# Kernel tuning notes

Measured on AMD Instinct MI355X. Metric: run time of the kernel, lower is better.

The kernel has to match this reference:

```python
import jax, jax.numpy as jnp
import numpy as np

NUM_CAPSULE = 10
DIM_CAPSULE = 16
NUM_ROUTING = 3
EPS = 1e-7  # tf.keras.backend.epsilon()


def squash(v, axis=-1):
    s2 = jnp.sum(jnp.square(v), axis=axis, keepdims=True)
    scale = s2 / (1.0 + s2) / jnp.sqrt(s2 + EPS)
    return scale * v


def setup_inputs() -> dict:
    key = jax.random.key(0)
    k1, k2 = jax.random.split(key)
    B, in_dim = 16384, 2048
    inputs = jax.random.normal(k1, (B, in_dim), dtype=jnp.float32)
    # glorot-uniform-ish scale for the kernel
    limit = np.sqrt(6.0 / (in_dim + NUM_CAPSULE * DIM_CAPSULE)).astype(np.float32)
    kernel = jax.random.uniform(k2, (in_dim, NUM_CAPSULE * DIM_CAPSULE),
                                dtype=jnp.float32, minval=-limit, maxval=limit)
    return {"inputs": inputs, "kernel": kernel}


def reference(inputs, kernel):
    B = inputs.shape[0]
    # [B, in_dim] @ [in_dim, nc*dc] -> [B, nc, dc]
    inputs_hat = (inputs @ kernel).reshape(B, NUM_CAPSULE, DIM_CAPSULE)
    b = jnp.zeros((B, NUM_CAPSULE, 1), dtype=inputs.dtype)
    outputs = None
    for _ in range(NUM_ROUTING):
        c = jax.nn.softmax(b, axis=1)                      # [B, nc, 1]
        s = jnp.sum(c * inputs_hat, axis=1, keepdims=True)  # [B, 1, dc]
        outputs = squash(s)                                 # [B, 1, dc]
        # matmul(inputs_hat, outputs, transpose_b=True) -> [B, nc, 1]
        b = b + jnp.einsum('bnd,bd->bn', inputs_hat, outputs[:, 0, :])[:, :, None]
    return outputs[:, 0, :]  # [B, dc]
```

## Files before the change

kernel.cpp:

```cpp
#include <hip/hip_runtime.h>

typedef unsigned int u32;
typedef unsigned short u16;
typedef __attribute__((ext_vector_type(8))) __bf16 bf16x8;
typedef __attribute__((ext_vector_type(4))) float f32x4;

#define N_CAP 10
#define D_CAP 16
#define NN 160
#define KK 2048
#define BM 64
#define NSTEPS 64
#define THREADS 704
#define HAT_STRIDE 165
#define BSTEP 20480
#define TILE_B 8192
#define NBUF 3

__device__ __align__(16) unsigned char Wpack_g[NSTEPS * BSTEP];

__device__ __forceinline__ u32 pack_hi(float f0, float f1) {
  u32 u0 = __builtin_bit_cast(u32, f0), u1 = __builtin_bit_cast(u32, f1);
  return (u0 >> 16) | (u1 & 0xFFFF0000u);
}
__device__ __forceinline__ float hi_part(float f) {
  u32 u = __builtin_bit_cast(u32, f) & 0xFFFF0000u;
  return __builtin_bit_cast(float, u);
}
union U4B8 { uint4 u; bf16x8 b; };

__device__ __forceinline__ void split2(const float4& x, const float4& y,
                                       bf16x8& h, bf16x8& l) {
  U4B8 hh, ll;
  hh.u.x = pack_hi(x.x, x.y); hh.u.y = pack_hi(x.z, x.w);
  hh.u.z = pack_hi(y.x, y.y); hh.u.w = pack_hi(y.z, y.w);
  float l0 = x.x - hi_part(x.x), l1 = x.y - hi_part(x.y);
  float l2 = x.z - hi_part(x.z), l3 = x.w - hi_part(x.w);
  float l4 = y.x - hi_part(y.x), l5 = y.y - hi_part(y.y);
  float l6 = y.z - hi_part(y.z), l7 = y.w - hi_part(y.w);
  ll.u.x = pack_hi(l0, l1); ll.u.y = pack_hi(l2, l3);
  ll.u.z = pack_hi(l4, l5); ll.u.w = pack_hi(l6, l7);
  h = hh.b; l = ll.b;
}

__global__ void pack_w(const float* __restrict__ W) {
  const int tid = blockIdx.x * 256 + threadIdx.x;
  if (tid >= NSTEPS * 5 * 64 * 4) return;
  const int v = tid & 3;
  const int lane = (tid >> 2) & 63;
  const int sw = tid >> 8;
  const int wjp = sw % 5;
  const int s = sw / 5;
  const int col = 32 * wjp + 16 * (v & 1) + (lane & 15);
  const int kb = 32 * s + 8 * (lane >> 4);
  u32 r[4];
#pragma unroll
  for (int jj = 0; jj < 4; ++jj) {
    float x0 = W[(size_t)(kb + 2 * jj) * NN + col];
    float x1 = W[(size_t)(kb + 2 * jj + 1) * NN + col];
    if (v >= 2) { x0 -= hi_part(x0); x1 -= hi_part(x1); }
    r[jj] = pack_hi(x0, x1);
  }
  uint4 o; o.x = r[0]; o.y = r[1]; o.z = r[2]; o.w = r[3];
  *(uint4*)(Wpack_g + (size_t)tid * 16) = o;
}

#define GLOAD(gp, lp) __builtin_amdgcn_global_load_lds( \
    (const __attribute__((address_space(1))) u32*)(gp), \
    (__attribute__((address_space(3))) u32*)(lp), 16, 0, 0)
#define BARRIER() asm volatile("s_barrier" ::: "memory")

__global__ __launch_bounds__(THREADS, 1) void capsule_fused(
    const float* __restrict__ X, float* __restrict__ out) {
  __shared__ __align__(16) char smem[BM * HAT_STRIDE * 4];
  char* As = smem;
  float* hat = (float*)smem;

  const int t = threadIdx.x;
  const int rbase = blockIdx.x * BM;
  const int lane = t & 63;
  const int w = t >> 6;

  if (w == 10) {
    const float* g0 = X + (size_t)(rbase + (lane >> 3)) * KK
                        + (size_t)(((lane & 7) ^ (lane >> 3)) * 4);
#define STAGE(sv, bv) do {                                        \
    const float* gs_ = g0 + (size_t)(sv) * 32;                    \
    char* lb_ = As + (bv) * TILE_B;                               \
    GLOAD(gs_,           lb_);                                    \
    GLOAD(gs_ +  8 * KK, lb_ + 1024);                             \
    GLOAD(gs_ + 16 * KK, lb_ + 2048);                             \
    GLOAD(gs_ + 24 * KK, lb_ + 3072);                             \
    GLOAD(gs_ + 32 * KK, lb_ + 4096);                             \
    GLOAD(gs_ + 40 * KK, lb_ + 5120);                             \
    GLOAD(gs_ + 48 * KK, lb_ + 6144);                             \
    GLOAD(gs_ + 56 * KK, lb_ + 7168);                             \
  } while (0)
    STAGE(0, 0);
    STAGE(1, 1);
    asm volatile("s_waitcnt vmcnt(8)" ::: "memory");
    BARRIER();
    int pj = 2;
#pragma unroll 1
    for (int s = 0; s < NSTEPS; ++s) {
      if (s + 2 < NSTEPS) {
        STAGE(s + 2, pj);
        asm volatile("s_waitcnt vmcnt(8)" ::: "memory");
      } else {
        asm volatile("s_waitcnt vmcnt(0)" ::: "memory");
      }
      BARRIER();
      pj = (pj == 2) ? 0 : pj + 1;
    }
#undef STAGE
  } else {
    const int wip = (w >= 5) ? 1 : 0;
    const int wjp = w - 5 * wip;
    const int l15 = lane & 15;
    const int q = lane >> 4;
    const int r0 = 32 * wip + l15;
    const int r1 = r0 + 16;
    const int c0 = 2 * q, c1 = 2 * q + 1;
    const int o00 = (r0 >> 3) * 1024 + (r0 & 7) * 128 + ((c0 ^ (r0 & 7)) << 4);
    const int o01 = (r0 >> 3) * 1024 + (r0 & 7) * 128 + ((c1 ^ (r0 & 7)) << 4);
    const int o10 = (r1 >> 3) * 1024 + (r1 & 7) * 128 + ((c0 ^ (r1 & 7)) << 4);
    const int o11 = (r1 >> 3) * 1024 + (r1 & 7) * 128 + ((c1 ^ (r1 & 7)) << 4);
    const unsigned char* pB = Wpack_g + ((size_t)(wjp * 64 + lane)) * 64;

    f32x4 acc00 = {0.f,0.f,0.f,0.f}, acc01 = {0.f,0.f,0.f,0.f};
    f32x4 acc10 = {0.f,0.f,0.f,0.f}, acc11 = {0.f,0.f,0.f,0.f};

    BARRIER();
    int ci = 0;
#pragma unroll 1
    for (int s = 0; s < NSTEPS; ++s) {
      const uint4* bp4 = (const uint4*)(pB + (size_t)s * BSTEP);
      uint4 B0 = bp4[0], B1 = bp4[1], B2 = bp4[2], B3 = bp4[3];
      const char* cb = As + ci * TILE_B;
      float4 A00 = *(const float4*)(cb + o00);
      float4 A01 = *(const float4*)(cb + o01);
      float4 A10 = *(const float4*)(cb + o10);
      float4 A11 = *(const float4*)(cb + o11);
      bf16x8 ah0, al0, ah1, al1;
      split2(A00, A01, ah0, al0);
      split2(A10, A11, ah1, al1);
      U4B8 ub0, ub1, ub2, ub3;
      ub0.u = B0; ub1.u = B1; ub2.u = B2; ub3.u = B3;
      acc00 = __builtin_amdgcn_mfma_f32_16x16x32_bf16(ah0, ub0.b, acc00, 0,0,0);
      acc00 = __builtin_amdgcn_mfma_f32_16x16x32_bf16(ah0, ub2.b, acc00, 0,0,0);
      acc00 = __builtin_amdgcn_mfma_f32_16x16x32_bf16(al0, ub0.b, acc00, 0,0,0);
      acc01 = __builtin_amdgcn_mfma_f32_16x16x32_bf16(ah0, ub1.b, acc01, 0,0,0);
      acc01 = __builtin_amdgcn_mfma_f32_16x16x32_bf16(ah0, ub3.b, acc01, 0,0,0);
      acc01 = __builtin_amdgcn_mfma_f32_16x16x32_bf16(al0, ub1.b, acc01, 0,0,0);
      acc10 = __builtin_amdgcn_mfma_f32_16x16x32_bf16(ah1, ub0.b, acc10, 0,0,0);
      acc10 = __builtin_amdgcn_mfma_f32_16x16x32_bf16(ah1, ub2.b, acc10, 0,0,0);
      acc10 = __builtin_amdgcn_mfma_f32_16x16x32_bf16(al1, ub0.b, acc10, 0,0,0);
      acc11 = __builtin_amdgcn_mfma_f32_16x16x32_bf16(ah1, ub1.b, acc11, 0,0,0);
      acc11 = __builtin_amdgcn_mfma_f32_16x16x32_bf16(ah1, ub3.b, acc11, 0,0,0);
      acc11 = __builtin_amdgcn_mfma_f32_16x16x32_bf16(al1, ub1.b, acc11, 0,0,0);
      BARRIER();
      ci = (ci == 2) ? 0 : ci + 1;
    }
#pragma unroll
    for (int r = 0; r < 4; ++r) {
      const int rowb = 32 * wip + 4 * q + r;
      const int colb = 32 * wjp + l15;
      hat[rowb * HAT_STRIDE + colb]             = acc00[r];
      hat[rowb * HAT_STRIDE + colb + 16]        = acc01[r];
      hat[(rowb + 16) * HAT_STRIDE + colb]      = acc10[r];
      hat[(rowb + 16) * HAT_STRIDE + colb + 16] = acc11[r];
    }
  }
  __syncthreads();

  if (t < BM * 8) {
    const int r = t >> 3;
    const int d0 = t & 7;
    float h0[N_CAP], h1[N_CAP];
#pragma unroll
    for (int n = 0; n < N_CAP; ++n) {
      h0[n] = hat[r * HAT_STRIDE + n * D_CAP + d0];
      h1[n] = hat[r * HAT_STRIDE + n * D_CAP + d0 + 8];
    }
    float bb[N_CAP];
#pragma unroll
    for (int n = 0; n < N_CAP; ++n) bb[n] = 0.f;
    float v0 = 0.f, v1 = 0.f;
#pragma unroll
    for (int it = 0; it < 3; ++it) {
      float mx = bb[0];
#pragma unroll
      for (int n = 1; n < N_CAP; ++n) mx = fmaxf(mx, bb[n]);
      float c[N_CAP], se = 0.f;
#pragma unroll
      for (int n = 0; n < N_CAP; ++n) { c[n] = __expf(bb[n] - mx); se += c[n]; }
      const float inv = 1.f / se;
      float s0 = 0.f, s1 = 0.f;
#pragma unroll
      for (int n = 0; n < N_CAP; ++n) { s0 += c[n] * h0[n]; s1 += c[n] * h1[n]; }
      s0 *= inv; s1 *= inv;
      float s2 = s0 * s0 + s1 * s1;
      s2 += __shfl_xor(s2, 1);
      s2 += __shfl_xor(s2, 2);
      s2 += __shfl_xor(s2, 4);
      const float scale = s2 / ((1.f + s2) * sqrtf(s2 + 1e-7f));
      v0 = scale * s0; v1 = scale * s1;
      if (it < 2) {
#pragma unroll
        for (int n = 0; n < N_CAP; ++n) {
          float dd = h0[n] * v0 + h1[n] * v1;
          dd += __shfl_xor(dd, 1);
          dd += __shfl_xor(dd, 2);
          dd += __shfl_xor(dd, 4);
          bb[n] += dd;
        }
      }
    }
    out[(size_t)(rbase + r) * D_CAP + d0] = v0;
    out[(size_t)(rbase + r) * D_CAP + d0 + 8] = v1;
  }
}

extern "C" void kernel_launch(void* const* d_in, const int* in_sizes, int n_in,
                              void* d_out, int out_size, void* d_ws, size_t ws_size,
                              hipStream_t stream) {
  const float* X = (const float*)d_in[0];
  const float* W = (const float*)d_in[1];
  if (n_in >= 2 && in_sizes[0] == KK * NN) {
    X = (const float*)d_in[1];
    W = (const float*)d_in[0];
  }
  (void)d_ws; (void)ws_size; (void)out_size;
  pack_w<<<(NSTEPS * 5 * 64 * 4 + 255) / 256, 256, 0, stream>>>(W);
  capsule_fused<<<16384 / BM, THREADS, 0, stream>>>(X, (float*)d_out);
}
```

Measured before the change: 239.4 us.

## Double K-step per barrier and register-prefetch packed weights one iteration ahead

```diff
diff --git a/kernel.cpp b/kernel.cpp
--- a/kernel.cpp
+++ b/kernel.cpp
@@ -11,10 +11,11 @@
 #define KK 2048
 #define BM 64
 #define NSTEPS 64
+#define NITER 32
 #define THREADS 704
 #define HAT_STRIDE 165
 #define BSTEP 20480
-#define TILE_B 8192
+#define TILE2 16384
 #define NBUF 3
 
 __device__ __align__(16) unsigned char Wpack_g[NSTEPS * BSTEP];
@@ -69,12 +70,13 @@
     (const __attribute__((address_space(1))) u32*)(gp), \
     (__attribute__((address_space(3))) u32*)(lp), 16, 0, 0)
 #define BARRIER() asm volatile("s_barrier" ::: "memory")
+#define BLOAD(dst, addr) \
+  asm volatile("global_load_dwordx4 %0, %1, off" : "=v"(dst) : "v"(addr))
 
 __global__ __launch_bounds__(THREADS, 1) void capsule_fused(
     const float* __restrict__ X, float* __restrict__ out) {
-  __shared__ __align__(16) char smem[BM * HAT_STRIDE * 4];
-  char* As = smem;
-  float* hat = (float*)smem;
+  __shared__ __align__(16) char As[NBUF * TILE2];
+  __shared__ __align__(16) float hat[BM * HAT_STRIDE];
 
   const int t = threadIdx.x;
   const int rbase = blockIdx.x * BM;
@@ -84,35 +86,45 @@
   if (w == 10) {
     const float* g0 = X + (size_t)(rbase + (lane >> 3)) * KK
                         + (size_t)(((lane & 7) ^ (lane >> 3)) * 4);
-#define STAGE(sv, bv) do {                                        \
-    const float* gs_ = g0 + (size_t)(sv) * 32;                    \
-    char* lb_ = As + (bv) * TILE_B;                               \
-    GLOAD(gs_,           lb_);                                    \
-    GLOAD(gs_ +  8 * KK, lb_ + 1024);                             \
-    GLOAD(gs_ + 16 * KK, lb_ + 2048);                             \
-    GLOAD(gs_ + 24 * KK, lb_ + 3072);                             \
-    GLOAD(gs_ + 32 * KK, lb_ + 4096);                             \
-    GLOAD(gs_ + 40 * KK, lb_ + 5120);                             \
-    GLOAD(gs_ + 48 * KK, lb_ + 6144);                             \
-    GLOAD(gs_ + 56 * KK, lb_ + 7168);                             \
+#define STAGE2(IT, BV) do {                                       \
+    const float* ga_ = g0 + (size_t)(2 * (IT)) * 32;              \
+    char* la_ = As + (BV) * TILE2;                                \
+    GLOAD(ga_,           la_);                                    \
+    GLOAD(ga_ +  8 * KK, la_ + 1024);                             \
+    GLOAD(ga_ + 16 * KK, la_ + 2048);                             \
+    GLOAD(ga_ + 24 * KK, la_ + 3072);                             \
+    GLOAD(ga_ + 32 * KK, la_ + 4096);                             \
+    GLOAD(ga_ + 40 * KK, la_ + 5120);                             \
+    GLOAD(ga_ + 48 * KK, la_ + 6144);                             \
+    GLOAD(ga_ + 56 * KK, la_ + 7168);                             \
+    const float* gb_ = ga_ + 32;                                  \
+    char* lb_ = la_ + 8192;                                       \
+    GLOAD(gb_,           lb_);                                    \
+    GLOAD(gb_ +  8 * KK, lb_ + 1024);                             \
+    GLOAD(gb_ + 16 * KK, lb_ + 2048);                             \
+    GLOAD(gb_ + 24 * KK, lb_ + 3072);                             \
+    GLOAD(gb_ + 32 * KK, lb_ + 4096);                             \
+    GLOAD(gb_ + 40 * KK, lb_ + 5120);                             \
+    GLOAD(gb_ + 48 * KK, lb_ + 6144);                             \
+    GLOAD(gb_ + 56 * KK, lb_ + 7168);                             \
   } while (0)
-    STAGE(0, 0);
-    STAGE(1, 1);
-    asm volatile("s_waitcnt vmcnt(8)" ::: "memory");
+    STAGE2(0, 0);
+    STAGE2(1, 1);
+    asm volatile("s_waitcnt vmcnt(16)" ::: "memory");
     BARRIER();
     int pj = 2;
 #pragma unroll 1
-    for (int s = 0; s < NSTEPS; ++s) {
-      if (s + 2 < NSTEPS) {
-        STAGE(s + 2, pj);
-        asm volatile("s_waitcnt vmcnt(8)" ::: "memory");
+    for (int i = 0; i < NITER; ++i) {
+      if (i + 2 < NITER) {
+        STAGE2(i + 2, pj);
+        asm volatile("s_waitcnt vmcnt(16)" ::: "memory");
       } else {
         asm volatile("s_waitcnt vmcnt(0)" ::: "memory");
       }
       BARRIER();
       pj = (pj == 2) ? 0 : pj + 1;
     }
-#undef STAGE
+#undef STAGE2
   } else {
     const int wip = (w >= 5) ? 1 : 0;
     const int wjp = w - 5 * wip;
@@ -125,42 +137,75 @@
     const int o01 = (r0 >> 3) * 1024 + (r0 & 7) * 128 + ((c1 ^ (r0 & 7)) << 4);
     const int o10 = (r1 >> 3) * 1024 + (r1 & 7) * 128 + ((c0 ^ (r1 & 7)) << 4);
     const int o11 = (r1 >> 3) * 1024 + (r1 & 7) * 128 + ((c1 ^ (r1 & 7)) << 4);
-    const unsigned char* pB = Wpack_g + ((size_t)(wjp * 64 + lane)) * 64;
+    const unsigned char* pBw = Wpack_g + ((size_t)(wjp * 64 + lane)) * 64;
 
     f32x4 acc00 = {0.f,0.f,0.f,0.f}, acc01 = {0.f,0.f,0.f,0.f};
     f32x4 acc10 = {0.f,0.f,0.f,0.f}, acc11 = {0.f,0.f,0.f,0.f};
 
+    uint4 Ba[8], Bb[8];
+    BLOAD(Ba[0], pBw);                BLOAD(Ba[1], pBw + 16);
+    BLOAD(Ba[2], pBw + 32);           BLOAD(Ba[3], pBw + 48);
+    BLOAD(Ba[4], pBw + BSTEP);        BLOAD(Ba[5], pBw + BSTEP + 16);
+    BLOAD(Ba[6], pBw + BSTEP + 32);   BLOAD(Ba[7], pBw + BSTEP + 48);
+
     BARRIER();
     int ci = 0;
+
+#define MFMA12(AH0, AL0, AH1, AL1, B0, B1, B2, B3)                               \
+    {                                                                            \
+      U4B8 u0, u1, u2, u3;                                                       \
+      u0.u = B0; u1.u = B1; u2.u = B2; u3.u = B3;                                \
+      acc00 = __builtin_amdgcn_mfma_f32_16x16x32_bf16(AH0, u0.b, acc00, 0,0,0);  \
+      acc00 = __builtin_amdgcn_mfma_f32_16x16x32_bf16(AH0, u2.b, acc00, 0,0,0);  \
+      acc00 = __builtin_amdgcn_mfma_f32_16x16x32_bf16(AL0, u0.b, acc00, 0,0,0);  \
+      acc01 = __builtin_amdgcn_mfma_f32_16x16x32_bf16(AH0, u1.b, acc01, 0,0,0);  \
+      acc01 = __builtin_amdgcn_mfma_f32_16x16x32_bf16(AH0, u3.b, acc01, 0,0,0);  \
+      acc01 = __builtin_amdgcn_mfma_f32_16x16x32_bf16(AL0, u1.b, acc01, 0,0,0);  \
+      acc10 = __builtin_amdgcn_mfma_f32_16x16x32_bf16(AH1, u0.b, acc10, 0,0,0);  \
+      acc10 = __builtin_amdgcn_mfma_f32_16x16x32_bf16(AH1, u2.b, acc10, 0,0,0);  \
+      acc10 = __builtin_amdgcn_mfma_f32_16x16x32_bf16(AL1, u0.b, acc10, 0,0,0);  \
+      acc11 = __builtin_amdgcn_mfma_f32_16x16x32_bf16(AH1, u1.b, acc11, 0,0,0);  \
+      acc11 = __builtin_amdgcn_mfma_f32_16x16x32_bf16(AH1, u3.b, acc11, 0,0,0);  \
+      acc11 = __builtin_amdgcn_mfma_f32_16x16x32_bf16(AL1, u1.b, acc11, 0,0,0);  \
+    }
+
+#define ITER(I, BC, BN)                                                          \
+    {                                                                            \
+      const char* cb = As + ci * TILE2;                                          \
+      float4 A00a = *(const float4*)(cb + o00);                                  \
+      float4 A01a = *(const float4*)(cb + o01);                                  \
+      float4 A10a = *(const float4*)(cb + o10);                                  \
+      float4 A11a = *(const float4*)(cb + o11);                                  \
+      float4 A00b = *(const float4*)(cb + 8192 + o00);                           \
+      float4 A01b = *(const float4*)(cb + 8192 + o01);                           \
+      float4 A10b = *(const float4*)(cb + 8192 + o10);                           \
+      float4 A11b = *(const float4*)(cb + 8192 + o11);                           \
+      const unsigned char* bp = pBw + (size_t)((((I) + 1) & (NITER - 1)) * 2) * BSTEP; \
+      BLOAD(BN[0], bp);              BLOAD(BN[1], bp + 16);                      \
+      BLOAD(BN[2], bp + 32);         BLOAD(BN[3], bp + 48);                      \
+      BLOAD(BN[4], bp + BSTEP);      BLOAD(BN[5], bp + BSTEP + 16);              \
+      BLOAD(BN[6], bp + BSTEP + 32); BLOAD(BN[7], bp + BSTEP + 48);              \
+      bf16x8 ah0a, al0a, ah1a, al1a, ah0b, al0b, ah1b, al1b;                     \
+      split2(A00a, A01a, ah0a, al0a);                                            \
+      split2(A10a, A11a, ah1a, al1a);                                            \
+      split2(A00b, A01b, ah0b, al0b);                                            \
+      split2(A10b, A11b, ah1b, al1b);                                            \
+      asm volatile("s_waitcnt vmcnt(8)" ::: "memory");           \
+      __builtin_amdgcn_sched_barrier(0);                                         \
+      MFMA12(ah0a, al0a, ah1a, al1a, BC[0], BC[1], BC[2], BC[3])                 \
+      MFMA12(ah0b, al0b, ah1b, al1b, BC[4], BC[5], BC[6], BC[7])                 \
+      BARRIER();                                                                 \
+      ci = (ci == 2) ? 0 : ci + 1;                                               \
+    }
+
 #pragma unroll 1
-    for (int s = 0; s < NSTEPS; ++s) {
-      const uint4* bp4 = (const uint4*)(pB + (size_t)s * BSTEP);
-      uint4 B0 = bp4[0], B1 = bp4[1], B2 = bp4[2], B3 = bp4[3];
-      const char* cb = As + ci * TILE_B;
-      float4 A00 = *(const float4*)(cb + o00);
-      float4 A01 = *(const float4*)(cb + o01);
-      float4 A10 = *(const float4*)(cb + o10);
-      float4 A11 = *(const float4*)(cb + o11);
-      bf16x8 ah0, al0, ah1, al1;
-      split2(A00, A01, ah0, al0);
-      split2(A10, A11, ah1, al1);
-      U4B8 ub0, ub1, ub2, ub3;
-      ub0.u = B0; ub1.u = B1; ub2.u = B2; ub3.u = B3;
-      acc00 = __builtin_amdgcn_mfma_f32_16x16x32_bf16(ah0, ub0.b, acc00, 0,0,0);
-      acc00 = __builtin_amdgcn_mfma_f32_16x16x32_bf16(ah0, ub2.b, acc00, 0,0,0);
-      acc00 = __builtin_amdgcn_mfma_f32_16x16x32_bf16(al0, ub0.b, acc00, 0,0,0);
-      acc01 = __builtin_amdgcn_mfma_f32_16x16x32_bf16(ah0, ub1.b, acc01, 0,0,0);
-      acc01 = __builtin_amdgcn_mfma_f32_16x16x32_bf16(ah0, ub3.b, acc01, 0,0,0);
-      acc01 = __builtin_amdgcn_mfma_f32_16x16x32_bf16(al0, ub1.b, acc01, 0,0,0);
-      acc10 = __builtin_amdgcn_mfma_f32_16x16x32_bf16(ah1, ub0.b, acc10, 0,0,0);
-      acc10 = __builtin_amdgcn_mfma_f32_16x16x32_bf16(ah1, ub2.b, acc10, 0,0,0);
-      acc10 = __builtin_amdgcn_mfma_f32_16x16x32_bf16(al1, ub0.b, acc10, 0,0,0);
-      acc11 = __builtin_amdgcn_mfma_f32_16x16x32_bf16(ah1, ub1.b, acc11, 0,0,0);
-      acc11 = __builtin_amdgcn_mfma_f32_16x16x32_bf16(ah1, ub3.b, acc11, 0,0,0);
-      acc11 = __builtin_amdgcn_mfma_f32_16x16x32_bf16(al1, ub1.b, acc11, 0,0,0);
-      BARRIER();
-      ci = (ci == 2) ? 0 : ci + 1;
-    }
+    for (int i = 0; i < NITER; i += 2) {
+      ITER(i,     Ba, Bb)
+      ITER(i + 1, Bb, Ba)
+    }
+#undef ITER
+#undef MFMA12
+
 #pragma unroll
     for (int r = 0; r < 4; ++r) {
       const int rowb = 32 * wip + 4 * q + r;
```

New measurement: 225.2 us. 1.06x faster.

## Stage packed weight tiles into LDS via producer wave async loads

Applied to the files above, without the earlier changes.

```diff
diff --git a/kernel.cpp b/kernel.cpp
--- a/kernel.cpp
+++ b/kernel.cpp
@@ -14,7 +14,7 @@
 #define THREADS 704
 #define HAT_STRIDE 165
 #define BSTEP 20480
-#define TILE_B 8192
+#define ATILE 8192
 #define NBUF 3
 
 __device__ __align__(16) unsigned char Wpack_g[NSTEPS * BSTEP];
@@ -43,14 +43,33 @@
   h = hh.b; l = ll.b;
 }
 
+__device__ __forceinline__ void mfma12(bf16x8 ah0, bf16x8 al0, bf16x8 ah1,
+                                       bf16x8 al1, bf16x8 bh0, bf16x8 bh1,
+                                       bf16x8 bl0, bf16x8 bl1, f32x4& a00,
+                                       f32x4& a01, f32x4& a10, f32x4& a11) {
+  a00 = __builtin_amdgcn_mfma_f32_16x16x32_bf16(ah0, bh0, a00, 0, 0, 0);
+  a00 = __builtin_amdgcn_mfma_f32_16x16x32_bf16(ah0, bl0, a00, 0, 0, 0);
+  a00 = __builtin_amdgcn_mfma_f32_16x16x32_bf16(al0, bh0, a00, 0, 0, 0);
+  a01 = __builtin_amdgcn_mfma_f32_16x16x32_bf16(ah0, bh1, a01, 0, 0, 0);
+  a01 = __builtin_amdgcn_mfma_f32_16x16x32_bf16(ah0, bl1, a01, 0, 0, 0);
+  a01 = __builtin_amdgcn_mfma_f32_16x16x32_bf16(al0, bh1, a01, 0, 0, 0);
+  a10 = __builtin_amdgcn_mfma_f32_16x16x32_bf16(ah1, bh0, a10, 0, 0, 0);
+  a10 = __builtin_amdgcn_mfma_f32_16x16x32_bf16(ah1, bl0, a10, 0, 0, 0);
+  a10 = __builtin_amdgcn_mfma_f32_16x16x32_bf16(al1, bh0, a10, 0, 0, 0);
+  a11 = __builtin_amdgcn_mfma_f32_16x16x32_bf16(ah1, bh1, a11, 0, 0, 0);
+  a11 = __builtin_amdgcn_mfma_f32_16x16x32_bf16(ah1, bl1, a11, 0, 0, 0);
+  a11 = __builtin_amdgcn_mfma_f32_16x16x32_bf16(al1, bh1, a11, 0, 0, 0);
+}
+
 __global__ void pack_w(const float* __restrict__ W) {
   const int tid = blockIdx.x * 256 + threadIdx.x;
-  if (tid >= NSTEPS * 5 * 64 * 4) return;
-  const int v = tid & 3;
-  const int lane = (tid >> 2) & 63;
-  const int sw = tid >> 8;
-  const int wjp = sw % 5;
-  const int s = sw / 5;
+  if (tid >= NSTEPS * 4 * 5 * 64) return;
+  const int lane = tid & 63;
+  const int rest = tid >> 6;
+  const int wjp = rest % 5;
+  const int rest2 = rest / 5;
+  const int v = rest2 & 3;
+  const int s = rest2 >> 2;
   const int col = 32 * wjp + 16 * (v & 1) + (lane & 15);
   const int kb = 32 * s + 8 * (lane >> 4);
   u32 r[4];
@@ -72,9 +91,9 @@
 
 __global__ __launch_bounds__(THREADS, 1) void capsule_fused(
     const float* __restrict__ X, float* __restrict__ out) {
-  __shared__ __align__(16) char smem[BM * HAT_STRIDE * 4];
-  char* As = smem;
-  float* hat = (float*)smem;
+  __shared__ __align__(16) char AsA[NBUF * ATILE];
+  __shared__ __align__(16) char AsB[NBUF * BSTEP];
+  __shared__ __align__(16) float hat[BM * HAT_STRIDE];
 
   const int t = threadIdx.x;
   const int rbase = blockIdx.x * BM;
@@ -84,28 +103,34 @@
   if (w == 10) {
     const float* g0 = X + (size_t)(rbase + (lane >> 3)) * KK
                         + (size_t)(((lane & 7) ^ (lane >> 3)) * 4);
-#define STAGE(sv, bv) do {                                        \
-    const float* gs_ = g0 + (size_t)(sv) * 32;                    \
-    char* lb_ = As + (bv) * TILE_B;                               \
-    GLOAD(gs_,           lb_);                                    \
-    GLOAD(gs_ +  8 * KK, lb_ + 1024);                             \
-    GLOAD(gs_ + 16 * KK, lb_ + 2048);                             \
-    GLOAD(gs_ + 24 * KK, lb_ + 3072);                             \
-    GLOAD(gs_ + 32 * KK, lb_ + 4096);                             \
-    GLOAD(gs_ + 40 * KK, lb_ + 5120);                             \
-    GLOAD(gs_ + 48 * KK, lb_ + 6144);                             \
-    GLOAD(gs_ + 56 * KK, lb_ + 7168);                             \
+    const unsigned char* gw0 = Wpack_g + (size_t)lane * 16;
+#define STAGE(S, BV) do {                                         \
+    const float* ga_ = g0 + (size_t)(S) * 32;                     \
+    char* la_ = AsA + (BV) * ATILE;                               \
+    GLOAD(ga_,           la_);                                    \
+    GLOAD(ga_ +  8 * KK, la_ + 1024);                             \
+    GLOAD(ga_ + 16 * KK, la_ + 2048);                             \
+    GLOAD(ga_ + 24 * KK, la_ + 3072);                             \
+    GLOAD(ga_ + 32 * KK, la_ + 4096);                             \
+    GLOAD(ga_ + 40 * KK, la_ + 5120);                             \
+    GLOAD(ga_ + 48 * KK, la_ + 6144);                             \
+    GLOAD(ga_ + 56 * KK, la_ + 7168);                             \
+    const unsigned char* gw_ = gw0 + (size_t)(S) * BSTEP;         \
+    char* lw_ = AsB + (BV) * BSTEP;                               \
+    _Pragma("unroll")                                             \
+    for (int c_ = 0; c_ < 20; ++c_)                               \
+      GLOAD(gw_ + c_ * 1024, lw_ + c_ * 1024);                    \
   } while (0)
     STAGE(0, 0);
     STAGE(1, 1);
-    asm volatile("s_waitcnt vmcnt(8)" ::: "memory");
+    asm volatile("s_waitcnt vmcnt(28)" ::: "memory");
     BARRIER();
     int pj = 2;
 #pragma unroll 1
-    for (int s = 0; s < NSTEPS; ++s) {
-      if (s + 2 < NSTEPS) {
-        STAGE(s + 2, pj);
-        asm volatile("s_waitcnt vmcnt(8)" ::: "memory");
+    for (int i = 0; i < NSTEPS; ++i) {
+      if (i + 2 < NSTEPS) {
+        STAGE(i + 2, pj);
+        asm volatile("s_waitcnt vmcnt(28)" ::: "memory");
       } else {
         asm volatile("s_waitcnt vmcnt(0)" ::: "memory");
       }
@@ -125,7 +150,7 @@
     const int o01 = (r0 >> 3) * 1024 + (r0 & 7) * 128 + ((c1 ^ (r0 & 7)) << 4);
     const int o10 = (r1 >> 3) * 1024 + (r1 & 7) * 128 + ((c0 ^ (r1 & 7)) << 4);
     const int o11 = (r1 >> 3) * 1024 + (r1 & 7) * 128 + ((c1 ^ (r1 & 7)) << 4);
-    const unsigned char* pB = Wpack_g + ((size_t)(wjp * 64 + lane)) * 64;
+    const int ob = wjp * 1024 + lane * 16;
 
     f32x4 acc00 = {0.f,0.f,0.f,0.f}, acc01 = {0.f,0.f,0.f,0.f};
     f32x4 acc10 = {0.f,0.f,0.f,0.f}, acc11 = {0.f,0.f,0.f,0.f};
@@ -133,34 +158,26 @@
     BARRIER();
     int ci = 0;
 #pragma unroll 1
-    for (int s = 0; s < NSTEPS; ++s) {
-      const uint4* bp4 = (const uint4*)(pB + (size_t)s * BSTEP);
-      uint4 B0 = bp4[0], B1 = bp4[1], B2 = bp4[2], B3 = bp4[3];
-      const char* cb = As + ci * TILE_B;
-      float4 A00 = *(const float4*)(cb + o00);
-      float4 A01 = *(const float4*)(cb + o01);
-      float4 A10 = *(const float4*)(cb + o10);
-      float4 A11 = *(const float4*)(cb + o11);
+    for (int i = 0; i < NSTEPS; ++i) {
+      const char* ca = AsA + ci * ATILE;
+      const char* cbb = AsB + ci * BSTEP + ob;
+      bf16x8 bh0 = *(const bf16x8*)(cbb);
+      bf16x8 bh1 = *(const bf16x8*)(cbb + 5120);
+      bf16x8 bl0 = *(const bf16x8*)(cbb + 10240);
+      bf16x8 bl1 = *(const bf16x8*)(cbb + 15360);
+      float4 A00 = *(const float4*)(ca + o00);
+      float4 A01 = *(const float4*)(ca + o01);
+      float4 A10 = *(const float4*)(ca + o10);
+      float4 A11 = *(const float4*)(ca + o11);
       bf16x8 ah0, al0, ah1, al1;
       split2(A00, A01, ah0, al0);
       split2(A10, A11, ah1, al1);
-      U4B8 ub0, ub1, ub2, ub3;
-      ub0.u = B0; ub1.u = B1; ub2.u = B2; ub3.u = B3;
-      acc00 = __builtin_amdgcn_mfma_f32_16x16x32_bf16(ah0, ub0.b, acc00, 0,0,0);
-      acc00 = __builtin_amdgcn_mfma_f32_16x16x32_bf16(ah0, ub2.b, acc00, 0,0,0);
-      acc00 = __builtin_amdgcn_mfma_f32_16x16x32_bf16(al0, ub0.b, acc00, 0,0,0);
-      acc01 = __builtin_amdgcn_mfma_f32_16x16x32_bf16(ah0, ub1.b, acc01, 0,0,0);
-      acc01 = __builtin_amdgcn_mfma_f32_16x16x32_bf16(ah0, ub3.b, acc01, 0,0,0);
-      acc01 = __builtin_amdgcn_mfma_f32_16x16x32_bf16(al0, ub1.b, acc01, 0,0,0);
-      acc10 = __builtin_amdgcn_mfma_f32_16x16x32_bf16(ah1, ub0.b, acc10, 0,0,0);
-      acc10 = __builtin_amdgcn_mfma_f32_16x16x32_bf16(ah1, ub2.b, acc10, 0,0,0);
-      acc10 = __builtin_amdgcn_mfma_f32_16x16x32_bf16(al1, ub0.b, acc10, 0,0,0);
-      acc11 = __builtin_amdgcn_mfma_f32_16x16x32_bf16(ah1, ub1.b, acc11, 0,0,0);
-      acc11 = __builtin_amdgcn_mfma_f32_16x16x32_bf16(ah1, ub3.b, acc11, 0,0,0);
-      acc11 = __builtin_amdgcn_mfma_f32_16x16x32_bf16(al1, ub1.b, acc11, 0,0,0);
+      mfma12(ah0, al0, ah1, al1, bh0, bh1, bl0, bl1,
+             acc00, acc01, acc10, acc11);
       BARRIER();
       ci = (ci == 2) ? 0 : ci + 1;
     }
+
 #pragma unroll
     for (int r = 0; r < 4; ++r) {
       const int rowb = 32 * wip + 4 * q + r;
@@ -231,6 +248,6 @@
     W = (const float*)d_in[0];
   }
   (void)d_ws; (void)ws_size; (void)out_size;
-  pack_w<<<(NSTEPS * 5 * 64 * 4 + 255) / 256, 256, 0, stream>>>(W);
+  pack_w<<<(NSTEPS * 4 * 5 * 64 + 255) / 256, 256, 0, stream>>>(W);
   capsule_fused<<<16384 / BM, THREADS, 0, stream>>>(X, (float*)d_out);
 }
```

New measurement: 208.3 us. 1.15x faster.
